# Performance work log

Measured on AMD Instinct MI355X. Metric: run time of the kernel, lower is better.

## Reference

```python
import jax, jax.numpy as jnp
import numpy as np

LAMBD = 1.0  # margin, matches init kwarg lambd
N, C, D = 16384, 4096, 128


def setup_inputs() -> dict:
    key = jax.random.key(0)
    k1, k2, k3 = jax.random.split(key, 3)
    embeddings = jax.random.normal(k1, (N, D), dtype=jnp.float32)
    targets = jax.random.randint(k2, (N,), 0, C, dtype=jnp.int64)
    centers = jax.random.normal(k3, (C, D), dtype=jnp.float32)
    return {"embeddings": embeddings, "targets": targets, "centers": centers}


def reference(embeddings, targets, centers):
    # Squared euclidean distances from every sample to every center, [n, C],
    # via ||e||^2 + ||c||^2 - 2 e.c (avoids the [n, C, d] broadcast tensor).
    e2 = jnp.sum(embeddings * embeddings, axis=-1, keepdims=True)          # [n, 1]
    c2 = jnp.sum(centers * centers, axis=-1)                               # [C]
    dist = e2 + c2[None, :] - 2.0 * jnp.matmul(embeddings, centers.T)      # [n, C]

    tgt = targets.astype(jnp.int32)
    ap = jnp.take_along_axis(dist, tgt[:, None], axis=1)                   # [n, 1]

    # loss_val[i, c] = lambd + d(e_i, center_{y_i}) - d(e_i, center_c)
    loss_val = LAMBD + ap - dist                                           # [n, C]

    # Triplet (i, y_i, c) is mined iff loss_val > 0 and c != y_i.
    not_label = jnp.arange(dist.shape[1], dtype=jnp.int32)[None, :] != tgt[:, None]
    mask = (loss_val > 0.0) & not_label

    # For mined triplets relu(ap - an + lambd) == loss_val (already > 0).
    total = jnp.sum(jnp.where(mask, loss_val, 0.0))
    cnt = jnp.sum(mask).astype(loss_val.dtype)
    # If no triplet violates the margin, the original returns 0.
    return jnp.where(cnt > 0.0, total / jnp.maximum(cnt, 1.0), 0.0)
```

## Files before the change

kernel.cpp:

```cpp
#include <hip/hip_runtime.h>

#define N_SAMP 16384
#define N_CENT 4096
#define DIM    128
#define LAMBD  1.0f
#define NSLOT  256

typedef _Float16 half8  __attribute__((ext_vector_type(8)));
typedef float    floatx4 __attribute__((ext_vector_type(4)));

struct Slot { float sum; unsigned int cnt; unsigned int pad[30]; };

__device__ __forceinline__ void gload_lds16(const void* g, void* l) {
  __builtin_amdgcn_global_load_lds(
      (__attribute__((address_space(1))) void*)(g),
      (__attribute__((address_space(3))) void*)(l), 16, 0, 0);
}

__global__ __launch_bounds__(256) void prep_kernel(
    const float* __restrict__ E, const float* __restrict__ Cc,
    const int* __restrict__ tgt,
    _Float16* __restrict__ Eh, _Float16* __restrict__ Ch,
    float* __restrict__ c2, float* __restrict__ rowk,
    Slot* __restrict__ slots) {
  const int tid = threadIdx.x;
  const int STAT_BLOCKS = (N_SAMP + N_CENT) / 4;
  if ((int)blockIdx.x < STAT_BLOCKS) {
    if (blockIdx.x == 0) { slots[tid].sum = 0.f; slots[tid].cnt = 0u; }
    const int wv   = blockIdx.x * 4 + (tid >> 6);
    const int lane = tid & 63;
    if (wv < N_SAMP) {
      const int yi = tgt[wv];
      float2 e = *(const float2*)(E  + (size_t)wv * DIM + lane * 2);
      float2 c = *(const float2*)(Cc + (size_t)yi * DIM + lane * 2);
      float s = c.x * (c.x - 2.f * e.x) + c.y * (c.y - 2.f * e.y);
      #pragma unroll
      for (int off = 32; off > 0; off >>= 1) s += __shfl_down(s, off);
      if (lane == 0) rowk[wv] = LAMBD + s;
    } else {
      const int cI = wv - N_SAMP;
      float2 c = *(const float2*)(Cc + (size_t)cI * DIM + lane * 2);
      float s = c.x * c.x + c.y * c.y;
      #pragma unroll
      for (int off = 32; off > 0; off >>= 1) s += __shfl_down(s, off);
      if (lane == 0) c2[cI] = s;
    }
  } else {
    const int t = ((int)blockIdx.x - STAT_BLOCKS) * 256 + tid;
    const int NE8 = N_SAMP * DIM / 8;
    const float4* src;
    half8* dst;
    int idx;
    if (t < NE8) { src = (const float4*)E;  dst = (half8*)Eh; idx = t; }
    else         { src = (const float4*)Cc; dst = (half8*)Ch; idx = t - NE8; }
    float4 a = src[(size_t)idx * 2], b = src[(size_t)idx * 2 + 1];
    half8 h;
    h[0]=(_Float16)a.x; h[1]=(_Float16)a.y; h[2]=(_Float16)a.z; h[3]=(_Float16)a.w;
    h[4]=(_Float16)b.x; h[5]=(_Float16)b.y; h[6]=(_Float16)b.z; h[7]=(_Float16)b.w;
    dst[idx] = h;
  }
}

__global__ __launch_bounds__(512, 2) void center_gemm_kernel(
    const _Float16* __restrict__ Eh, const _Float16* __restrict__ Ch,
    const float* __restrict__ c2, const float* __restrict__ rowk,
    const int* __restrict__ tgt,
    Slot* __restrict__ slots) {
  __shared__ _Float16 As[2][128 * DIM];
  __shared__ _Float16 Bs[256 * DIM];
  __shared__ float c2S[256];
  __shared__ float rowkS[2][128];
  __shared__ int   yS[2][128];
  __shared__ float swsum[8];
  __shared__ int   swcnt[8];

  const int tid  = threadIdx.x;
  const int w    = tid >> 6;
  const int lane = tid & 63;

  const int bid    = blockIdx.x;
  const int xcd    = bid & 7;
  const int j      = bid >> 3;
  const int bm_grp = xcd * 2 + (j & 1);
  const int bn_grp = j >> 1;
  const int bn0    = bn_grp * 256;

  const int p  = lane & 15;
  const int r4 = lane >> 4;

  {
    const char* gB = (const char*)(Ch + (size_t)bn0 * DIM);
    char* lB = (char*)Bs;
    #pragma unroll
    for (int it = 0; it < 8; ++it) {
      const int chunk = w * 8 + it;
      const int row   = chunk * 4 + r4;
      gload_lds16(gB + row * 256 + (p ^ (row & 15)) * 16, lB + chunk * 1024);
    }
    const char* gA = (const char*)(Eh + (size_t)bm_grp * 8 * 128 * DIM);
    char* lA = (char*)As[0];
    #pragma unroll
    for (int it = 0; it < 4; ++it) {
      const int chunk = w * 4 + it;
      const int row   = chunk * 4 + r4;
      gload_lds16(gA + row * 256 + (p ^ (row & 15)) * 16, lA + chunk * 1024);
    }
  }
  if (tid < 256) c2S[tid] = c2[bn0 + tid];
  if (tid < 128) {
    const int rg0 = bm_grp * 8 * 128 + tid;
    rowkS[0][tid] = rowk[rg0];
    yS[0][tid]    = tgt[rg0];
  }
  __syncthreads();

  const int wm = w >> 2, wn = w & 3;
  const int q = lane >> 4, r = lane & 15;
  const int row0 = wm * 64, col0 = wn * 64;

  float lsum = 0.f;
  int   lcnt = 0;

  for (int t = 0; t < 8; ++t) {
    const int cur = t & 1;

    if (t < 7) {
      const char* gA = (const char*)(Eh + (size_t)(bm_grp * 8 + t + 1) * 128 * DIM);
      char* lA = (char*)As[cur ^ 1];
      #pragma unroll
      for (int it = 0; it < 4; ++it) {
        const int chunk = w * 4 + it;
        const int row   = chunk * 4 + r4;
        gload_lds16(gA + row * 256 + (p ^ (row & 15)) * 16, lA + chunk * 1024);
      }
      if (tid < 128) {
        const int rg1 = (bm_grp * 8 + t + 1) * 128 + tid;
        rowkS[cur ^ 1][tid] = rowk[rg1];
        yS[cur ^ 1][tid]    = tgt[rg1];
      }
    }

    floatx4 acc[4][4];
    #pragma unroll
    for (int a = 0; a < 4; ++a)
      #pragma unroll
      for (int b = 0; b < 4; ++b)
        acc[a][b] = (floatx4){0.f, 0.f, 0.f, 0.f};

    #pragma unroll
    for (int ks = 0; ks < 4; ++ks) {
      const int cidx = ks * 4 + q;
      half8 af[4], bf[4];
      #pragma unroll
      for (int mt = 0; mt < 4; ++mt)
        af[mt] = *(const half8*)&As[cur][(row0 + mt * 16 + r) * DIM + ((cidx ^ r) * 8)];
      #pragma unroll
      for (int nt = 0; nt < 4; ++nt)
        bf[nt] = *(const half8*)&Bs[(col0 + nt * 16 + r) * DIM + ((cidx ^ r) * 8)];
      #pragma unroll
      for (int mt = 0; mt < 4; ++mt)
        #pragma unroll
        for (int nt = 0; nt < 4; ++nt)
          acc[mt][nt] = __builtin_amdgcn_mfma_f32_16x16x32_f16(af[mt], bf[nt], acc[mt][nt], 0, 0, 0);
    }

    #pragma unroll
    for (int mt = 0; mt < 4; ++mt) {
      float rk[4]; int yv[4];
      #pragma unroll
      for (int rg = 0; rg < 4; ++rg) {
        const int row = row0 + mt * 16 + q * 4 + rg;
        rk[rg] = rowkS[cur][row];
        yv[rg] = yS[cur][row];
      }
      #pragma unroll
      for (int nt = 0; nt < 4; ++nt) {
        const int col  = col0 + nt * 16 + r;
        const float c2v = c2S[col];
        const int gcol = bn0 + col;
        #pragma unroll
        for (int rg = 0; rg < 4; ++rg) {
          const float v = rk[rg] + 2.f * acc[mt][nt][rg] - c2v;
          const bool mined = (v > 0.f) & (gcol != yv[rg]);
          lsum += mined ? v : 0.f;
          lcnt += mined ? 1 : 0;
        }
      }
    }

    __syncthreads();
  }

  #pragma unroll
  for (int off = 32; off > 0; off >>= 1) {
    lsum += __shfl_down(lsum, off);
    lcnt += __shfl_down(lcnt, off);
  }
  if (lane == 0) { swsum[w] = lsum; swcnt[w] = lcnt; }
  __syncthreads();
  if (tid == 0) {
    float s = 0.f; int c = 0;
    #pragma unroll
    for (int k = 0; k < 8; ++k) { s += swsum[k]; c += swcnt[k]; }
    Slot* sl = &slots[bid & (NSLOT - 1)];
    atomicAdd(&sl->sum, s);
    atomicAdd(&sl->cnt, (unsigned int)c);
  }
}

__global__ __launch_bounds__(256) void finalize_kernel(
    const Slot* __restrict__ slots, float* __restrict__ out) {
  const int tid = threadIdx.x;
  float s = slots[tid].sum;
  unsigned int c = slots[tid].cnt;
  #pragma unroll
  for (int off = 32; off > 0; off >>= 1) {
    s += __shfl_down(s, off);
    c += __shfl_down(c, off);
  }
  __shared__ float ss[4];
  __shared__ unsigned int sc[4];
  if ((tid & 63) == 0) { ss[tid >> 6] = s; sc[tid >> 6] = c; }
  __syncthreads();
  if (tid == 0) {
    const float S = ss[0] + ss[1] + ss[2] + ss[3];
    const unsigned int C = sc[0] + sc[1] + sc[2] + sc[3];
    out[0] = (C > 0u) ? (S / (float)C) : 0.f;
  }
}

__global__ void zero_kernel(float* ws_sum, unsigned int* ws_cnt) {
  if (threadIdx.x == 0) { *ws_sum = 0.f; *ws_cnt = 0u; }
}

__global__ void finalize_simple(const float* __restrict__ ws_sum,
                                const unsigned int* __restrict__ ws_cnt,
                                float* __restrict__ out) {
  if (threadIdx.x == 0 && blockIdx.x == 0) {
    const unsigned int c = *ws_cnt;
    out[0] = (c > 0u) ? (*ws_sum / (float)c) : 0.f;
  }
}

__global__ __launch_bounds__(256) void fallback_kernel(
    const float* __restrict__ E, const float* __restrict__ Cc,
    const int* __restrict__ tgt,
    float* __restrict__ ws_sum, unsigned int* __restrict__ ws_cnt) {
  __shared__ float eS[DIM];
  __shared__ float apS;
  const int i = blockIdx.x;
  const int tid = threadIdx.x;
  if (tid < DIM) eS[tid] = E[(size_t)i * DIM + tid];
  __syncthreads();
  const int yi = tgt[i];
  float dloc[16];
  #pragma unroll
  for (int j = 0; j < 16; ++j) {
    const int c = tid + 256 * j;
    const float* cp = Cc + (size_t)c * DIM;
    float s = 0.f;
    for (int d = 0; d < DIM; d += 4) {
      float4 cv = *(const float4*)(cp + d);
      s += cv.x * (cv.x - 2.f * eS[d + 0]) + cv.y * (cv.y - 2.f * eS[d + 1])
         + cv.z * (cv.z - 2.f * eS[d + 2]) + cv.w * (cv.w - 2.f * eS[d + 3]);
    }
    dloc[j] = s;
    if (c == yi) apS = s;
  }
  __syncthreads();
  const float apv = apS;
  float lsum = 0.f; int lcnt = 0;
  #pragma unroll
  for (int j = 0; j < 16; ++j) {
    const int c = tid + 256 * j;
    const float v = LAMBD + apv - dloc[j];
    const bool mined = (v > 0.f) & (c != yi);
    lsum += mined ? v : 0.f;
    lcnt += mined ? 1 : 0;
  }
  #pragma unroll
  for (int off = 32; off > 0; off >>= 1) {
    lsum += __shfl_down(lsum, off);
    lcnt += __shfl_down(lcnt, off);
  }
  __shared__ float swsum[4];
  __shared__ int   swcnt[4];
  const int w = tid >> 6, lane = tid & 63;
  if (lane == 0) { swsum[w] = lsum; swcnt[w] = lcnt; }
  __syncthreads();
  if (tid == 0) {
    atomicAdd(ws_sum, swsum[0] + swsum[1] + swsum[2] + swsum[3]);
    atomicAdd(ws_cnt, (unsigned int)(swcnt[0] + swcnt[1] + swcnt[2] + swcnt[3]));
  }
}

extern "C" void kernel_launch(void* const* d_in, const int* in_sizes, int n_in,
                              void* d_out, int out_size, void* d_ws, size_t ws_size,
                              hipStream_t stream) {
  const float* E   = (const float*)d_in[0];
  const int*   tgt = (const int*)d_in[1];
  const float* Cc  = (const float*)d_in[2];
  float* out = (float*)d_out;

  const size_t EH_BYTES = (size_t)N_SAMP * DIM * 2;
  const size_t CH_BYTES = (size_t)N_CENT * DIM * 2;
  const size_t C2_BYTES = (size_t)N_CENT * 4;
  const size_t RK_BYTES = (size_t)N_SAMP * 4;
  const size_t SL_BYTES = (size_t)NSLOT * sizeof(Slot);
  const size_t NEEDED = EH_BYTES + CH_BYTES + C2_BYTES + RK_BYTES + SL_BYTES;

  char* ws = (char*)d_ws;
  if (ws_size >= NEEDED) {
    _Float16* Eh = (_Float16*)ws;
    _Float16* Ch = (_Float16*)(ws + EH_BYTES);
    float* c2    = (float*)(ws + EH_BYTES + CH_BYTES);
    float* rowk  = (float*)(ws + EH_BYTES + CH_BYTES + C2_BYTES);
    Slot* slots  = (Slot*)(ws + EH_BYTES + CH_BYTES + C2_BYTES + RK_BYTES);

    const int STAT_BLOCKS = (N_SAMP + N_CENT) / 4;
    const int CONV_BLOCKS = (N_SAMP * DIM / 8 + N_CENT * DIM / 8) / 256;
    prep_kernel<<<STAT_BLOCKS + CONV_BLOCKS, 256, 0, stream>>>(
        E, Cc, tgt, Eh, Ch, c2, rowk, slots);
    center_gemm_kernel<<<256, 512, 0, stream>>>(Eh, Ch, c2, rowk, tgt, slots);
    finalize_kernel<<<1, 256, 0, stream>>>(slots, out);
  } else {
    float* ws_sum = (float*)ws;
    unsigned int* ws_cnt = (unsigned int*)(ws_sum + 1);
    zero_kernel<<<1, 64, 0, stream>>>(ws_sum, ws_cnt);
    fallback_kernel<<<N_SAMP, 256, 0, stream>>>(E, Cc, tgt, ws_sum, ws_cnt);
    finalize_simple<<<1, 64, 0, stream>>>(ws_sum, ws_cnt, out);
  }
}
```

Before: 94.79 us.

## Fuse prep passes, fold bias into MFMA accumulator, drop label mask and finalize launch

The prep kernel now reads each row once, computing the row statistic and writing the fp16 copy in the same pass. It also pre-scales E by 2 so the GEMM accumulator can start at rowk - c2 instead of being rescaled afterwards. B fragments are kept in registers across all M tiles, and the per-element label check is removed: the positive term is counted unconditionally and then corrected by subtracting N*lambda and N, since the label column always contributes exactly lambda. The mined count uses a wave ballot and popcount. The separate finalize kernel is replaced by a last-block ticket reduction, which removes one launch but adds atomics and fence overhead. The label-column correction assumes fp16 rounding yields a positive value there, and the 2*E scaling changes fp16 precision slightly.

```diff
diff --git a/kernel.cpp b/kernel.cpp
--- a/kernel.cpp
+++ b/kernel.cpp
@@ -6,6 +6,7 @@
 #define LAMBD  1.0f
 #define NSLOT  256
 
+typedef _Float16 half4v __attribute__((ext_vector_type(4)));
 typedef _Float16 half8  __attribute__((ext_vector_type(8)));
 typedef float    floatx4 __attribute__((ext_vector_type(4)));
 
@@ -23,56 +24,54 @@
     _Float16* __restrict__ Eh, _Float16* __restrict__ Ch,
     float* __restrict__ c2, float* __restrict__ rowk,
     Slot* __restrict__ slots) {
-  const int tid = threadIdx.x;
-  const int STAT_BLOCKS = (N_SAMP + N_CENT) / 4;
-  if ((int)blockIdx.x < STAT_BLOCKS) {
-    if (blockIdx.x == 0) { slots[tid].sum = 0.f; slots[tid].cnt = 0u; }
-    const int wv   = blockIdx.x * 4 + (tid >> 6);
-    const int lane = tid & 63;
-    if (wv < N_SAMP) {
-      const int yi = tgt[wv];
-      float2 e = *(const float2*)(E  + (size_t)wv * DIM + lane * 2);
-      float2 c = *(const float2*)(Cc + (size_t)yi * DIM + lane * 2);
-      float s = c.x * (c.x - 2.f * e.x) + c.y * (c.y - 2.f * e.y);
-      #pragma unroll
-      for (int off = 32; off > 0; off >>= 1) s += __shfl_down(s, off);
-      if (lane == 0) rowk[wv] = LAMBD + s;
-    } else {
-      const int cI = wv - N_SAMP;
-      float2 c = *(const float2*)(Cc + (size_t)cI * DIM + lane * 2);
-      float s = c.x * c.x + c.y * c.y;
-      #pragma unroll
-      for (int off = 32; off > 0; off >>= 1) s += __shfl_down(s, off);
-      if (lane == 0) c2[cI] = s;
-    }
+  const int tid  = threadIdx.x;
+  const int w    = tid >> 6;
+  const int lane = tid & 63;
+  const int l    = lane & 31;
+  const int E_BLOCKS = N_SAMP / 8;
+
+  if ((int)blockIdx.x < E_BLOCKS) {
+    if (blockIdx.x == 0) {
+      slots[tid].sum = 0.f; slots[tid].cnt = 0u; slots[tid].pad[0] = 0u;
+    }
+    const int wv = blockIdx.x * 4 + w;
+    const int r0 = wv * 2 + (lane >> 5);
+    float4 e = *(const float4*)(E + (size_t)r0 * DIM + l * 4);
+    const int yi = tgt[r0];
+    float4 c = *(const float4*)(Cc + (size_t)yi * DIM + l * 4);
+    float s = c.x * (c.x - 2.f * e.x) + c.y * (c.y - 2.f * e.y)
+            + c.z * (c.z - 2.f * e.z) + c.w * (c.w - 2.f * e.w);
+    #pragma unroll
+    for (int off = 16; off > 0; off >>= 1) s += __shfl_xor(s, off);
+    if (l == 0) rowk[r0] = LAMBD + s;
+    half4v h;
+    h[0] = (_Float16)(2.f * e.x); h[1] = (_Float16)(2.f * e.y);
+    h[2] = (_Float16)(2.f * e.z); h[3] = (_Float16)(2.f * e.w);
+    *(half4v*)(Eh + (size_t)r0 * DIM + l * 4) = h;
   } else {
-    const int t = ((int)blockIdx.x - STAT_BLOCKS) * 256 + tid;
-    const int NE8 = N_SAMP * DIM / 8;
-    const float4* src;
-    half8* dst;
-    int idx;
-    if (t < NE8) { src = (const float4*)E;  dst = (half8*)Eh; idx = t; }
-    else         { src = (const float4*)Cc; dst = (half8*)Ch; idx = t - NE8; }
-    float4 a = src[(size_t)idx * 2], b = src[(size_t)idx * 2 + 1];
-    half8 h;
-    h[0]=(_Float16)a.x; h[1]=(_Float16)a.y; h[2]=(_Float16)a.z; h[3]=(_Float16)a.w;
-    h[4]=(_Float16)b.x; h[5]=(_Float16)b.y; h[6]=(_Float16)b.z; h[7]=(_Float16)b.w;
-    dst[idx] = h;
+    const int wv = ((int)blockIdx.x - E_BLOCKS) * 4 + w;
+    const int r0 = wv * 2 + (lane >> 5);
+    float4 c = *(const float4*)(Cc + (size_t)r0 * DIM + l * 4);
+    float s = c.x * c.x + c.y * c.y + c.z * c.z + c.w * c.w;
+    #pragma unroll
+    for (int off = 16; off > 0; off >>= 1) s += __shfl_xor(s, off);
+    if (l == 0) c2[r0] = s;
+    half4v h;
+    h[0] = (_Float16)c.x; h[1] = (_Float16)c.y;
+    h[2] = (_Float16)c.z; h[3] = (_Float16)c.w;
+    *(half4v*)(Ch + (size_t)r0 * DIM + l * 4) = h;
   }
 }
 
 __global__ __launch_bounds__(512, 2) void center_gemm_kernel(
     const _Float16* __restrict__ Eh, const _Float16* __restrict__ Ch,
     const float* __restrict__ c2, const float* __restrict__ rowk,
-    const int* __restrict__ tgt,
-    Slot* __restrict__ slots) {
+    Slot* __restrict__ slots, float* __restrict__ out) {
   __shared__ _Float16 As[2][128 * DIM];
   __shared__ _Float16 Bs[256 * DIM];
-  __shared__ float c2S[256];
-  __shared__ float rowkS[2][128];
-  __shared__ int   yS[2][128];
   __shared__ float swsum[8];
-  __shared__ int   swcnt[8];
+  __shared__ unsigned int swcnt[8];
+  __shared__ int tktS;
 
   const int tid  = threadIdx.x;
   const int w    = tid >> 6;
@@ -106,20 +105,32 @@
       gload_lds16(gA + row * 256 + (p ^ (row & 15)) * 16, lA + chunk * 1024);
     }
   }
-  if (tid < 256) c2S[tid] = c2[bn0 + tid];
-  if (tid < 128) {
-    const int rg0 = bm_grp * 8 * 128 + tid;
-    rowkS[0][tid] = rowk[rg0];
-    yS[0][tid]    = tgt[rg0];
-  }
-  __syncthreads();
 
   const int wm = w >> 2, wn = w & 3;
   const int q = lane >> 4, r = lane & 15;
   const int row0 = wm * 64, col0 = wn * 64;
 
+  float c2v[4];
+  #pragma unroll
+  for (int nt = 0; nt < 4; ++nt) c2v[nt] = c2[bn0 + col0 + nt * 16 + r];
+
+  const float* rkbase = rowk + bm_grp * 8 * 128;
+  floatx4 rkc[4], rkn[4];
+  #pragma unroll
+  for (int mt = 0; mt < 4; ++mt)
+    rkc[mt] = *(const floatx4*)(rkbase + row0 + mt * 16 + q * 4);
+
+  __syncthreads();
+
+  half8 bf[4][4];
+  #pragma unroll
+  for (int nt = 0; nt < 4; ++nt)
+    #pragma unroll
+    for (int ks = 0; ks < 4; ++ks)
+      bf[nt][ks] = *(const half8*)&Bs[(col0 + nt * 16 + r) * DIM + (((ks * 4 + q) ^ r) * 8)];
+
   float lsum = 0.f;
-  int   lcnt = 0;
+  unsigned int cntU = 0u;
 
   for (int t = 0; t < 8; ++t) {
     const int cur = t & 1;
@@ -133,99 +144,87 @@
         const int row   = chunk * 4 + r4;
         gload_lds16(gA + row * 256 + (p ^ (row & 15)) * 16, lA + chunk * 1024);
       }
-      if (tid < 128) {
-        const int rg1 = (bm_grp * 8 + t + 1) * 128 + tid;
-        rowkS[cur ^ 1][tid] = rowk[rg1];
-        yS[cur ^ 1][tid]    = tgt[rg1];
-      }
+      #pragma unroll
+      for (int mt = 0; mt < 4; ++mt)
+        rkn[mt] = *(const floatx4*)(rkbase + (t + 1) * 128 + row0 + mt * 16 + q * 4);
     }
 
     floatx4 acc[4][4];
     #pragma unroll
-    for (int a = 0; a < 4; ++a)
-      #pragma unroll
-      for (int b = 0; b < 4; ++b)
-        acc[a][b] = (floatx4){0.f, 0.f, 0.f, 0.f};
+    for (int mt = 0; mt < 4; ++mt)
+      #pragma unroll
+      for (int nt = 0; nt < 4; ++nt)
+        acc[mt][nt] = rkc[mt] - c2v[nt];
 
     #pragma unroll
     for (int ks = 0; ks < 4; ++ks) {
       const int cidx = ks * 4 + q;
-      half8 af[4], bf[4];
+      half8 af[4];
       #pragma unroll
       for (int mt = 0; mt < 4; ++mt)
         af[mt] = *(const half8*)&As[cur][(row0 + mt * 16 + r) * DIM + ((cidx ^ r) * 8)];
-      #pragma unroll
-      for (int nt = 0; nt < 4; ++nt)
-        bf[nt] = *(const half8*)&Bs[(col0 + nt * 16 + r) * DIM + ((cidx ^ r) * 8)];
       #pragma unroll
       for (int mt = 0; mt < 4; ++mt)
         #pragma unroll
         for (int nt = 0; nt < 4; ++nt)
-          acc[mt][nt] = __builtin_amdgcn_mfma_f32_16x16x32_f16(af[mt], bf[nt], acc[mt][nt], 0, 0, 0);
-    }
-
-    #pragma unroll
-    for (int mt = 0; mt < 4; ++mt) {
-      float rk[4]; int yv[4];
-      #pragma unroll
-      for (int rg = 0; rg < 4; ++rg) {
-        const int row = row0 + mt * 16 + q * 4 + rg;
-        rk[rg] = rowkS[cur][row];
-        yv[rg] = yS[cur][row];
-      }
+          acc[mt][nt] = __builtin_amdgcn_mfma_f32_16x16x32_f16(af[mt], bf[nt][ks], acc[mt][nt], 0, 0, 0);
+    }
+
+    #pragma unroll
+    for (int mt = 0; mt < 4; ++mt)
       #pragma unroll
       for (int nt = 0; nt < 4; ++nt) {
-        const int col  = col0 + nt * 16 + r;
-        const float c2v = c2S[col];
-        const int gcol = bn0 + col;
+        const floatx4 a = acc[mt][nt];
         #pragma unroll
         for (int rg = 0; rg < 4; ++rg) {
-          const float v = rk[rg] + 2.f * acc[mt][nt][rg] - c2v;
-          const bool mined = (v > 0.f) & (gcol != yv[rg]);
-          lsum += mined ? v : 0.f;
-          lcnt += mined ? 1 : 0;
+          const float v = a[rg];
+          lsum += fmaxf(v, 0.f);
+          cntU += (unsigned int)__popcll(__ballot(v > 0.f));
         }
       }
-    }
 
     __syncthreads();
-  }
-
-  #pragma unroll
-  for (int off = 32; off > 0; off >>= 1) {
-    lsum += __shfl_down(lsum, off);
-    lcnt += __shfl_down(lcnt, off);
-  }
-  if (lane == 0) { swsum[w] = lsum; swcnt[w] = lcnt; }
+    #pragma unroll
+    for (int mt = 0; mt < 4; ++mt) rkc[mt] = rkn[mt];
+  }
+
+  #pragma unroll
+  for (int off = 32; off > 0; off >>= 1) lsum += __shfl_down(lsum, off);
+  if (lane == 0) { swsum[w] = lsum; swcnt[w] = cntU; }
   __syncthreads();
   if (tid == 0) {
-    float s = 0.f; int c = 0;
+    float s = 0.f; unsigned int c = 0u;
     #pragma unroll
     for (int k = 0; k < 8; ++k) { s += swsum[k]; c += swcnt[k]; }
-    Slot* sl = &slots[bid & (NSLOT - 1)];
+    Slot* sl = &slots[bid];
     atomicAdd(&sl->sum, s);
-    atomicAdd(&sl->cnt, (unsigned int)c);
-  }
-}
-
-__global__ __launch_bounds__(256) void finalize_kernel(
-    const Slot* __restrict__ slots, float* __restrict__ out) {
-  const int tid = threadIdx.x;
-  float s = slots[tid].sum;
-  unsigned int c = slots[tid].cnt;
-  #pragma unroll
-  for (int off = 32; off > 0; off >>= 1) {
-    s += __shfl_down(s, off);
-    c += __shfl_down(c, off);
-  }
-  __shared__ float ss[4];
-  __shared__ unsigned int sc[4];
-  if ((tid & 63) == 0) { ss[tid >> 6] = s; sc[tid >> 6] = c; }
-  __syncthreads();
-  if (tid == 0) {
-    const float S = ss[0] + ss[1] + ss[2] + ss[3];
-    const unsigned int C = sc[0] + sc[1] + sc[2] + sc[3];
-    out[0] = (C > 0u) ? (S / (float)C) : 0.f;
+    atomicAdd(&sl->cnt, c);
+    __threadfence();
+    tktS = (int)atomicAdd(&slots[0].pad[0], 1u);
+  }
+  __syncthreads();
+
+  if (tktS == NSLOT - 1) {
+    float s = 0.f; unsigned int c = 0u;
+    if (tid < NSLOT) {
+      s = atomicAdd(&slots[tid].sum, 0.f);
+      c = atomicAdd(&slots[tid].cnt, 0u);
+    }
+    #pragma unroll
+    for (int off = 32; off > 0; off >>= 1) {
+      s += __shfl_down(s, off);
+      c += __shfl_down(c, off);
+    }
+    if (lane == 0) { swsum[w] = s; swcnt[w] = c; }
+    __syncthreads();
+    if (tid == 0) {
+      float S = 0.f; unsigned int C = 0u;
+      #pragma unroll
+      for (int k = 0; k < 8; ++k) { S += swsum[k]; C += swcnt[k]; }
+      const float Sc = S - (float)N_SAMP * LAMBD;
+      const long long Cc2 = (long long)C - (long long)N_SAMP;
+      out[0] = (Cc2 > 0) ? (Sc / (float)Cc2) : 0.f;
+    }
   }
 }
 
@@ -317,12 +316,11 @@
     float* rowk  = (float*)(ws + EH_BYTES + CH_BYTES + C2_BYTES);
     Slot* slots  = (Slot*)(ws + EH_BYTES + CH_BYTES + C2_BYTES + RK_BYTES);
 
-    const int STAT_BLOCKS = (N_SAMP + N_CENT) / 4;
-    const int CONV_BLOCKS = (N_SAMP * DIM / 8 + N_CENT * DIM / 8) / 256;
-    prep_kernel<<<STAT_BLOCKS + CONV_BLOCKS, 256, 0, stream>>>(
+    const int E_BLOCKS = N_SAMP / 8;
+    const int C_BLOCKS = N_CENT / 8;
+    prep_kernel<<<E_BLOCKS + C_BLOCKS, 256, 0, stream>>>(
         E, Cc, tgt, Eh, Ch, c2, rowk, slots);
-    center_gemm_kernel<<<256, 512, 0, stream>>>(Eh, Ch, c2, rowk, tgt, slots);
-    finalize_kernel<<<1, 256, 0, stream>>>(slots, out);
+    center_gemm_kernel<<<256, 512, 0, stream>>>(Eh, Ch, c2, rowk, slots, out);
   } else {
     float* ws_sum = (float*)ws;
     unsigned int* ws_cnt = (unsigned int*)(ws_sum + 1);
```

Result: no change. 96.43 us (+1.7%).
